# Kernel tuning notes

Hardware: AMD Instinct MI355X
Metric: run time of the kernel (lower is better)

The kernel has to match this reference:

```python
import jax, jax.numpy as jnp
import numpy as np

IN_FEATURES = 2048
OUT_FEATURES = 8192


def setup_inputs() -> dict:
    key = jax.random.key(0)
    k_x, k_w, k_s, k_b = jax.random.split(key, 4)
    x = jax.random.normal(k_x, (4, 2048, IN_FEATURES), dtype=jnp.float32)
    # int8 weights as produced by quantize(): values in [-128, 127]
    weight_int8 = jax.random.randint(k_w, (OUT_FEATURES, IN_FEATURES), -128, 128, dtype=jnp.int8)
    # per-output-row scale, shape [out_features, 1]
    scale = jax.random.uniform(k_s, (OUT_FEATURES, 1), dtype=jnp.float32, minval=1e-4, maxval=0.02)
    bias = jax.random.normal(k_b, (OUT_FEATURES,), dtype=jnp.float32) * 0.01
    return {"x": x, "weight_int8": weight_int8, "scale": scale, "bias": bias}


def reference(x, weight_int8, scale, bias):
    # dequantize: [out, in] int8 -> x.dtype, scaled per output row
    weight = weight_int8.astype(x.dtype) * scale.astype(x.dtype)
    # F.linear: x @ weight.T + bias
    return jnp.einsum('bsi,oi->bso', x, weight) + bias.astype(x.dtype)
```

## Files before the change

kernel.cpp:

```cpp
#include <hip/hip_runtime.h>
#include <hip/hip_bf16.h>

#define M_DIM 8192
#define N_DIM 8192
#define K_DIM 2048

#define BK 64
#define NT (K_DIM / BK)
#define SLOT_BYTES 16384

typedef float f32x4 __attribute__((ext_vector_type(4)));
typedef int   i32x4 __attribute__((ext_vector_type(4)));
typedef unsigned int u32;
typedef u32 u32x2 __attribute__((ext_vector_type(2)));
typedef u32 u32x4 __attribute__((ext_vector_type(4)));


__device__ __forceinline__ void gload16(const unsigned char* g, char* l) {
    __builtin_amdgcn_global_load_lds(
        (const __attribute__((address_space(1))) u32*)g,
        (__attribute__((address_space(3))) u32*)l, 16, 0, 0);
}

__device__ __forceinline__ u32 pack4(int a, int b, int c, int d) {
    return (u32)(a & 255) | ((u32)(b & 255) << 8) |
           ((u32)(c & 255) << 16) | ((u32)(d & 255) << 24);
}


__global__ void __launch_bounds__(256) quant_x_k(const float* __restrict__ x,
                                                 unsigned char* __restrict__ xq,
                                                 float* __restrict__ sx) {
    const int row = blockIdx.x;
    const int t = threadIdx.x;
    const float* xr = x + (size_t)row * K_DIM;
    f32x4 v0 = *((const f32x4*)xr + t * 2);
    f32x4 v1 = *((const f32x4*)xr + t * 2 + 1);
    float m = fabsf(v0[0]);
    m = fmaxf(m, fabsf(v0[1])); m = fmaxf(m, fabsf(v0[2])); m = fmaxf(m, fabsf(v0[3]));
    m = fmaxf(m, fabsf(v1[0])); m = fmaxf(m, fabsf(v1[1]));
    m = fmaxf(m, fabsf(v1[2])); m = fmaxf(m, fabsf(v1[3]));
#pragma unroll
    for (int off = 32; off >= 1; off >>= 1)
        m = fmaxf(m, __shfl_xor(m, off, 64));
    __shared__ float wmax[4];
    if ((t & 63) == 0) wmax[t >> 6] = m;
    __syncthreads();
    m = fmaxf(fmaxf(wmax[0], wmax[1]), fmaxf(wmax[2], wmax[3]));
    m = fmaxf(m, 1e-20f);
    const float rs = 127.0f / m;
    u32x2 o;
    o[0] = pack4((int)rintf(v0[0] * rs), (int)rintf(v0[1] * rs),
                 (int)rintf(v0[2] * rs), (int)rintf(v0[3] * rs));
    o[1] = pack4((int)rintf(v1[0] * rs), (int)rintf(v1[1] * rs),
                 (int)rintf(v1[2] * rs), (int)rintf(v1[3] * rs));
    *((u32x2*)(xq + (size_t)row * K_DIM) + t) = o;
    if (t == 0) sx[row] = m / 127.0f;
}


__global__ void __launch_bounds__(256) cvt_w_k(const int* __restrict__ w,
                                               unsigned char* __restrict__ Bt) {
    const int g = blockIdx.x;
    const int t = threadIdx.x;
    const int fr = t >> 4;
    const int kc = t & 15;
    const int col = g * 16 + fr;
    const int* wr = w + (size_t)col * K_DIM + kc * 128;

#pragma unroll
    for (int kk = 0; kk < 8; ++kk) {
        const int k = kc * 128 + kk * 16;
        const int kt = k >> 6;
        const int s4 = (k >> 4) & 3;
        u32x4 o;
#pragma unroll
        for (int j = 0; j < 4; ++j) {
            i32x4 a = *(const i32x4*)(wr + kk * 16 + j * 4);
            o[j] = pack4(a[0], a[1], a[2], a[3]);
        }
        *(u32x4*)(Bt + (size_t)g * 32768 + kt * 1024 + (s4 * 16 + fr) * 16) = o;
    }
}


__global__ void __launch_bounds__(512, 2)
gemm_i8(const unsigned char* __restrict__ Aq, const unsigned char* __restrict__ Bt,
        const float* __restrict__ sx, const float* __restrict__ sw,
        const float* __restrict__ bias, float* __restrict__ C) {
    extern __shared__ __align__(16) char ldsb[];

    const int bid = blockIdx.x;
    const int swz = (bid & 7) * 128 + (bid >> 3);
    const int rowBase = (swz >> 5) * 256;
    const int colBase = (swz & 31) * 256;

    const int t = threadIdx.x;
    const int l = t & 63;
    const int w = t >> 6;
    const int wm = w >> 2;
    const int wn = w & 3;
    const int fr = l & 15;
    const int s4 = l >> 4;

    const int sr = t >> 2;
    const int sk = (((t & 3) ^ ((sr >> 1) & 3)) * 16);
    const unsigned char* gA0 = Aq + (size_t)(rowBase + sr) * K_DIM + sk;
    const unsigned char* gA1 = Aq + (size_t)(rowBase + 128 + sr) * K_DIM + sk;

#define STAGE_A(tk) do { \
        char* _b = ldsb + ((tk) % 5) * SLOT_BYTES; \
        const int _k = (tk) * BK; \
        gload16(gA0 + _k, _b + t * 16); \
        gload16(gA1 + _k, _b + 8192 + t * 16); \
    } while (0)

    const unsigned char* bB[4];
#pragma unroll
    for (int ni = 0; ni < 4; ++ni)
        bB[ni] = Bt + (size_t)(colBase / 16 + wn * 4 + ni) * 32768 + l * 16;

#define BLOAD(dst, T) do { \
        _Pragma("unroll") \
        for (int ni = 0; ni < 4; ++ni) \
            dst[ni] = *(const i32x4*)(bB[ni] + (T) * 1024); \
    } while (0)

    const int pc = ((s4 ^ ((fr >> 1) & 3)) * 16);
    int aoff[8];
#pragma unroll
    for (int mi = 0; mi < 8; ++mi)
        aoff[mi] = (wm * 128 + mi * 16 + fr) * 64 + pc;

    i32x4 acc[8][4] = {};
    i32x4 afC[8], bf0[4], bf1[4];

#define SBF   __builtin_amdgcn_sched_barrier(0)
#define BAR   __builtin_amdgcn_s_barrier()
#define LGKM0 asm volatile("s_waitcnt lgkmcnt(0)" ::: "memory")
#define VM12  asm volatile("s_waitcnt vmcnt(12)" ::: "memory")
#define VM8   asm volatile("s_waitcnt vmcnt(8)" ::: "memory")
#define VM4   asm volatile("s_waitcnt vmcnt(4)" ::: "memory")
#define VM0   asm volatile("s_waitcnt vmcnt(0)" ::: "memory")

#define READS_A(slot) do { \
        const char* _s = ldsb + (slot) * SLOT_BYTES; \
        _Pragma("unroll") \
        for (int mi = 0; mi < 8; ++mi) afC[mi] = *(const i32x4*)(_s + aoff[mi]); \
    } while (0)

#define MFMA_ILV(BREG, NSLOT) do { \
        const char* _n = ldsb + (NSLOT) * SLOT_BYTES; \
        _Pragma("unroll") \
        for (int mi = 0; mi < 8; ++mi) { \
            _Pragma("unroll") \
            for (int ni = 0; ni < 4; ++ni) \
                acc[mi][ni] = __builtin_amdgcn_mfma_i32_16x16x64_i8( \
                    afC[mi], BREG[ni], acc[mi][ni], 0, 0, 0); \
            afC[mi] = *(const i32x4*)(_n + aoff[mi]); \
        } \
    } while (0)

#define MFMA_ALL(BREG) do { \
        _Pragma("unroll") \
        for (int mi = 0; mi < 8; ++mi) \
            _Pragma("unroll") \
            for (int ni = 0; ni < 4; ++ni) \
                acc[mi][ni] = __builtin_amdgcn_mfma_i32_16x16x64_i8( \
                    afC[mi], BREG[ni], acc[mi][ni], 0, 0, 0); \
    } while (0)

#define SBODY(T, DOSTG, VMMID) do { \
        VM4; LGKM0; SBF; BAR; SBF; \
        if (DOSTG) { STAGE_A((T) + 4); STAGE_A((T) + 5); } \
        MFMA_ILV(bf0, ((T) + 1) % 5); \
        BLOAD(bf0, (T) + 2); \
        VMMID; LGKM0; SBF; \
        MFMA_ILV(bf1, ((T) + 2) % 5); \
        BLOAD(bf1, (T) + 3); \
    } while (0)

    STAGE_A(0); STAGE_A(1); STAGE_A(2); STAGE_A(3);
    BLOAD(bf0, 0); BLOAD(bf1, 1);
    VM12; SBF; BAR; SBF;
    READS_A(0);

    SBODY(0,  true, VM8);  SBODY(2,  true, VM8);  SBODY(4,  true, VM8);
    SBODY(6,  true, VM8);  SBODY(8,  true, VM8);  SBODY(10, true, VM8);
    SBODY(12, true, VM8);  SBODY(14, true, VM8);  SBODY(16, true, VM8);
    SBODY(18, true, VM8);  SBODY(20, true, VM8);  SBODY(22, true, VM8);
    SBODY(24, true, VM8);  SBODY(26, true, VM8);
    SBODY(28, false, VM4);

    VM4; LGKM0; SBF;
    MFMA_ILV(bf0, 31 % 5);
    VM0; LGKM0; SBF;
    MFMA_ALL(bf1);

#undef SBODY
#undef MFMA_ALL
#undef MFMA_ILV
#undef READS_A
#undef BLOAD
#undef STAGE_A

#pragma unroll
    for (int ni = 0; ni < 4; ++ni) {
        const int col = colBase + wn * 64 + ni * 16 + fr;
        const float swc = sw[col];
        const float bz = bias[col];
#pragma unroll
        for (int mi = 0; mi < 8; ++mi) {
            const int rb = rowBase + wm * 128 + mi * 16 + s4 * 4;
            i32x4 a = acc[mi][ni];
#pragma unroll
            for (int r = 0; r < 4; ++r)
                C[(size_t)(rb + r) * N_DIM + col] =
                    (float)a[r] * (sx[rb + r] * swc) + bz;
        }
    }
}


typedef int i32x4_t __attribute__((ext_vector_type(4)));
__global__ void __launch_bounds__(256) naive_k(const float* __restrict__ x,
                                               const int* __restrict__ w,
                                               const float* __restrict__ scale,
                                               const float* __restrict__ bias,
                                               float* __restrict__ out) {
    __shared__ float xs[K_DIM];
    const int m = blockIdx.x >> 5;
    const int n = ((blockIdx.x & 31) << 8) + threadIdx.x;
    for (int i = threadIdx.x; i < K_DIM; i += 256) xs[i] = x[(size_t)m * K_DIM + i];
    __syncthreads();
    const int* wr = w + (size_t)n * K_DIM;
    float acc = 0.f;
    for (int k = 0; k < K_DIM; k += 4) {
        i32x4_t v = *(const i32x4_t*)(wr + k);
        acc += xs[k]     * (float)v[0];
        acc += xs[k + 1] * (float)v[1];
        acc += xs[k + 2] * (float)v[2];
        acc += xs[k + 3] * (float)v[3];
    }
    out[(size_t)m * N_DIM + n] = acc * scale[n] + bias[n];
}


extern "C" void kernel_launch(void* const* d_in, const int* in_sizes, int n_in,
                              void* d_out, int out_size, void* d_ws, size_t ws_size,
                              hipStream_t stream) {
    const float* x     = (const float*)d_in[0];
    const int*   w8    = (const int*)d_in[1];
    const float* sw    = (const float*)d_in[2];
    const float* bias  = (const float*)d_in[3];
    float*       out   = (float*)d_out;

    const size_t xq_bytes = (size_t)M_DIM * K_DIM;
    const size_t wq_bytes = (size_t)N_DIM * K_DIM;
    const size_t need = xq_bytes + wq_bytes + (size_t)M_DIM * sizeof(float);
    if (ws_size >= need) {
        unsigned char* xq = (unsigned char*)d_ws;
        unsigned char* Bt = xq + xq_bytes;
        float* sx = (float*)(Bt + wq_bytes);
        hipFuncSetAttribute((const void*)gemm_i8,
                            hipFuncAttributeMaxDynamicSharedMemorySize, 5 * SLOT_BYTES);
        quant_x_k<<<M_DIM, 256, 0, stream>>>(x, xq, sx);
        cvt_w_k<<<N_DIM / 16, 256, 0, stream>>>(w8, Bt);
        gemm_i8<<<dim3((M_DIM / 256) * (N_DIM / 256)), 512, 5 * SLOT_BYTES, stream>>>(
            xq, Bt, sx, sw, bias, out);
    } else {
        naive_k<<<(M_DIM * (N_DIM / 256)), 256, 0, stream>>>(x, w8, sw, bias, out);
    }
}
```

Baseline: 204.1 us.

## Give each wave private double-buffered LDS for A and drop block barriers

```diff
diff --git a/kernel.cpp b/kernel.cpp
--- a/kernel.cpp
+++ b/kernel.cpp
@@ -7,7 +7,8 @@
 
 #define BK 64
 #define NT (K_DIM / BK)
-#define SLOT_BYTES 16384
+#define WSLOT 8192
+#define WLDS  16384
 
 typedef float f32x4 __attribute__((ext_vector_type(4)));
 typedef int   i32x4 __attribute__((ext_vector_type(4)));
@@ -103,16 +104,18 @@
     const int fr = l & 15;
     const int s4 = l >> 4;
 
-    const int sr = t >> 2;
-    const int sk = (((t & 3) ^ ((sr >> 1) & 3)) * 16);
-    const unsigned char* gA0 = Aq + (size_t)(rowBase + sr) * K_DIM + sk;
-    const unsigned char* gA1 = Aq + (size_t)(rowBase + 128 + sr) * K_DIM + sk;
-
-#define STAGE_A(tk) do { \
-        char* _b = ldsb + ((tk) % 5) * SLOT_BYTES; \
+    char* ldsw = ldsb + w * WLDS;
+
+    const unsigned char* gAw = Aq +
+        (size_t)(rowBase + wm * 128 + (l >> 2)) * K_DIM +
+        (((l & 3) ^ ((l >> 3) & 3)) * 16);
+
+#define STAGE_W(tk) do { \
+        char* _b = ldsw + ((tk) & 1) * WSLOT; \
         const int _k = (tk) * BK; \
-        gload16(gA0 + _k, _b + t * 16); \
-        gload16(gA1 + _k, _b + 8192 + t * 16); \
+        _Pragma("unroll") \
+        for (int i = 0; i < 8; ++i) \
+            gload16(gAw + (size_t)(i * 16) * K_DIM + _k, _b + i * 1024 + l * 16); \
     } while (0)
 
     const unsigned char* bB[4];
@@ -130,27 +133,25 @@
     int aoff[8];
 #pragma unroll
     for (int mi = 0; mi < 8; ++mi)
-        aoff[mi] = (wm * 128 + mi * 16 + fr) * 64 + pc;
+        aoff[mi] = (mi * 16 + fr) * 64 + pc;
 
     i32x4 acc[8][4] = {};
     i32x4 afC[8], bf0[4], bf1[4];
 
 #define SBF   __builtin_amdgcn_sched_barrier(0)
-#define BAR   __builtin_amdgcn_s_barrier()
 #define LGKM0 asm volatile("s_waitcnt lgkmcnt(0)" ::: "memory")
 #define VM12  asm volatile("s_waitcnt vmcnt(12)" ::: "memory")
-#define VM8   asm volatile("s_waitcnt vmcnt(8)" ::: "memory")
 #define VM4   asm volatile("s_waitcnt vmcnt(4)" ::: "memory")
 #define VM0   asm volatile("s_waitcnt vmcnt(0)" ::: "memory")
 
 #define READS_A(slot) do { \
-        const char* _s = ldsb + (slot) * SLOT_BYTES; \
+        const char* _s = ldsw + (slot) * WSLOT; \
         _Pragma("unroll") \
         for (int mi = 0; mi < 8; ++mi) afC[mi] = *(const i32x4*)(_s + aoff[mi]); \
     } while (0)
 
 #define MFMA_ILV(BREG, NSLOT) do { \
-        const char* _n = ldsb + (NSLOT) * SLOT_BYTES; \
+        const char* _n = ldsw + (NSLOT) * WSLOT; \
         _Pragma("unroll") \
         for (int mi = 0; mi < 8; ++mi) { \
             _Pragma("unroll") \
@@ -170,39 +171,40 @@
                     afC[mi], BREG[ni], acc[mi][ni], 0, 0, 0); \
     } while (0)
 
-#define SBODY(T, DOSTG, VMMID) do { \
-        VM4; LGKM0; SBF; BAR; SBF; \
-        if (DOSTG) { STAGE_A((T) + 4); STAGE_A((T) + 5); } \
-        MFMA_ILV(bf0, ((T) + 1) % 5); \
-        BLOAD(bf0, (T) + 2); \
-        VMMID; LGKM0; SBF; \
-        MFMA_ILV(bf1, ((T) + 2) % 5); \
-        BLOAD(bf1, (T) + 3); \
-    } while (0)
-
-    STAGE_A(0); STAGE_A(1); STAGE_A(2); STAGE_A(3);
-    BLOAD(bf0, 0); BLOAD(bf1, 1);
-    VM12; SBF; BAR; SBF;
+#define ITER(T, BC) do { \
+        LGKM0; SBF; \
+        STAGE_W((T) + 2); \
+        VM12; SBF; \
+        MFMA_ILV(BC, ((T) + 1) & 1); \
+        BLOAD(BC, (T) + 2); \
+        VM12; SBF; \
+    } while (0)
+
+    STAGE_W(0);
+    BLOAD(bf0, 0);
+    STAGE_W(1);
+    BLOAD(bf1, 1);
+    VM12; SBF;
     READS_A(0);
 
-    SBODY(0,  true, VM8);  SBODY(2,  true, VM8);  SBODY(4,  true, VM8);
-    SBODY(6,  true, VM8);  SBODY(8,  true, VM8);  SBODY(10, true, VM8);
-    SBODY(12, true, VM8);  SBODY(14, true, VM8);  SBODY(16, true, VM8);
-    SBODY(18, true, VM8);  SBODY(20, true, VM8);  SBODY(22, true, VM8);
-    SBODY(24, true, VM8);  SBODY(26, true, VM8);
-    SBODY(28, false, VM4);
-
-    VM4; LGKM0; SBF;
-    MFMA_ILV(bf0, 31 % 5);
+#pragma unroll
+    for (int p = 0; p < 15; ++p) {
+        ITER(2 * p,     bf0);
+        ITER(2 * p + 1, bf1);
+    }
+
+    LGKM0; SBF;
+    VM4; SBF;
+    MFMA_ILV(bf0, 1);
     VM0; LGKM0; SBF;
     MFMA_ALL(bf1);
 
-#undef SBODY
+#undef ITER
 #undef MFMA_ALL
 #undef MFMA_ILV
 #undef READS_A
 #undef BLOAD
-#undef STAGE_A
+#undef STAGE_W
 
 #pragma unroll
     for (int ni = 0; ni < 4; ++ni) {
@@ -263,10 +265,10 @@
         unsigned char* Bt = xq + xq_bytes;
         float* sx = (float*)(Bt + wq_bytes);
         hipFuncSetAttribute((const void*)gemm_i8,
-                            hipFuncAttributeMaxDynamicSharedMemorySize, 5 * SLOT_BYTES);
+                            hipFuncAttributeMaxDynamicSharedMemorySize, 8 * WLDS);
         quant_x_k<<<M_DIM, 256, 0, stream>>>(x, xq, sx);
         cvt_w_k<<<N_DIM / 16, 256, 0, stream>>>(w8, Bt);
-        gemm_i8<<<dim3((M_DIM / 256) * (N_DIM / 256)), 512, 5 * SLOT_BYTES, stream>>>(
+        gemm_i8<<<dim3((M_DIM / 256) * (N_DIM / 256)), 512, 8 * WLDS, stream>>>(
             xq, Bt, sx, sw, bias, out);
     } else {
         naive_k<<<(M_DIM * (N_DIM / 256)), 256, 0, stream>>>(x, w8, sw, bias, out);
```

After: 251.5 us. +23.2%, slower.

## Deepen A-tile LDS ring to 8 slots and barrier once per four K-steps

Applied to the files above, without the earlier changes.

```diff
diff --git a/kernel.cpp b/kernel.cpp
--- a/kernel.cpp
+++ b/kernel.cpp
@@ -109,7 +109,7 @@
     const unsigned char* gA1 = Aq + (size_t)(rowBase + 128 + sr) * K_DIM + sk;
 
 #define STAGE_A(tk) do { \
-        char* _b = ldsb + ((tk) % 5) * SLOT_BYTES; \
+        char* _b = ldsb + ((tk) & 7) * SLOT_BYTES; \
         const int _k = (tk) * BK; \
         gload16(gA0 + _k, _b + t * 16); \
         gload16(gA1 + _k, _b + 8192 + t * 16); \
@@ -139,6 +139,7 @@
 #define BAR   __builtin_amdgcn_s_barrier()
 #define LGKM0 asm volatile("s_waitcnt lgkmcnt(0)" ::: "memory")
 #define VM12  asm volatile("s_waitcnt vmcnt(12)" ::: "memory")
+#define VM10  asm volatile("s_waitcnt vmcnt(10)" ::: "memory")
 #define VM8   asm volatile("s_waitcnt vmcnt(8)" ::: "memory")
 #define VM4   asm volatile("s_waitcnt vmcnt(4)" ::: "memory")
 #define VM0   asm volatile("s_waitcnt vmcnt(0)" ::: "memory")
@@ -170,34 +171,48 @@
                     afC[mi], BREG[ni], acc[mi][ni], 0, 0, 0); \
     } while (0)
 
-#define SBODY(T, DOSTG, VMMID) do { \
+#define SBODY4(T, STG4, VMM1) do { \
         VM4; LGKM0; SBF; BAR; SBF; \
-        if (DOSTG) { STAGE_A((T) + 4); STAGE_A((T) + 5); } \
-        MFMA_ILV(bf0, ((T) + 1) % 5); \
+        STAGE_A((T) + 5); STAGE_A((T) + 6); STAGE_A((T) + 7); \
+        if (STG4) STAGE_A((T) + 8); \
+        MFMA_ILV(bf0, ((T) + 1) & 7); \
         BLOAD(bf0, (T) + 2); \
-        VMMID; LGKM0; SBF; \
-        MFMA_ILV(bf1, ((T) + 2) % 5); \
+        VMM1; SBF; \
+        MFMA_ILV(bf1, ((T) + 2) & 7); \
         BLOAD(bf1, (T) + 3); \
-    } while (0)
-
-    STAGE_A(0); STAGE_A(1); STAGE_A(2); STAGE_A(3);
+        VM4; SBF; \
+        MFMA_ILV(bf0, ((T) + 3) & 7); \
+        BLOAD(bf0, (T) + 4); \
+        VM4; SBF; \
+        MFMA_ILV(bf1, ((T) + 4) & 7); \
+        BLOAD(bf1, (T) + 5); \
+    } while (0)
+
+    STAGE_A(0); STAGE_A(1); STAGE_A(2); STAGE_A(3); STAGE_A(4);
     BLOAD(bf0, 0); BLOAD(bf1, 1);
-    VM12; SBF; BAR; SBF;
+    VM8; SBF; BAR; SBF;
     READS_A(0);
 
-    SBODY(0,  true, VM8);  SBODY(2,  true, VM8);  SBODY(4,  true, VM8);
-    SBODY(6,  true, VM8);  SBODY(8,  true, VM8);  SBODY(10, true, VM8);
-    SBODY(12, true, VM8);  SBODY(14, true, VM8);  SBODY(16, true, VM8);
-    SBODY(18, true, VM8);  SBODY(20, true, VM8);  SBODY(22, true, VM8);
-    SBODY(24, true, VM8);  SBODY(26, true, VM8);
-    SBODY(28, false, VM4);
-
-    VM4; LGKM0; SBF;
-    MFMA_ILV(bf0, 31 % 5);
+    SBODY4(0,  true,  VM12);
+    SBODY4(4,  true,  VM12);
+    SBODY4(8,  true,  VM12);
+    SBODY4(12, true,  VM12);
+    SBODY4(16, true,  VM12);
+    SBODY4(20, true,  VM12);
+    SBODY4(24, false, VM10);
+
+    VM4; LGKM0; SBF; BAR; SBF;
+    MFMA_ILV(bf0, 29 & 7);
+    BLOAD(bf0, 30);
+    VM4; SBF;
+    MFMA_ILV(bf1, 30 & 7);
+    BLOAD(bf1, 31);
+    VM4; SBF;
+    MFMA_ILV(bf0, 31 & 7);
     VM0; LGKM0; SBF;
     MFMA_ALL(bf1);
 
-#undef SBODY
+#undef SBODY4
 #undef MFMA_ALL
 #undef MFMA_ILV
 #undef READS_A
@@ -263,10 +278,10 @@
         unsigned char* Bt = xq + xq_bytes;
         float* sx = (float*)(Bt + wq_bytes);
         hipFuncSetAttribute((const void*)gemm_i8,
-                            hipFuncAttributeMaxDynamicSharedMemorySize, 5 * SLOT_BYTES);
+                            hipFuncAttributeMaxDynamicSharedMemorySize, 8 * SLOT_BYTES);
         quant_x_k<<<M_DIM, 256, 0, stream>>>(x, xq, sx);
         cvt_w_k<<<N_DIM / 16, 256, 0, stream>>>(w8, Bt);
-        gemm_i8<<<dim3((M_DIM / 256) * (N_DIM / 256)), 512, 5 * SLOT_BYTES, stream>>>(
+        gemm_i8<<<dim3((M_DIM / 256) * (N_DIM / 256)), 512, 8 * SLOT_BYTES, stream>>>(
             xq, Bt, sx, sw, bias, out);
     } else {
         naive_k<<<(M_DIM * (N_DIM / 256)), 256, 0, stream>>>(x, w8, sw, bias, out);
```

Result: slower. 258.3 us (+26.6%).
